# Performance work log

Measured on AMD Instinct MI355X. Metric: run time of the kernel, lower is better.

Reference implementation:

```python
import jax, jax.numpy as jnp
import numpy as np

B, T, D = 4096, 200, 64
H1, H2 = 64, 32


def _prelu(x, a):
    # PReLU with a single learnable slope (torch default num_parameters=1)
    return jnp.where(x >= 0, x, a * x)


def setup_inputs() -> dict:
    key = jax.random.key(0)
    ks = jax.random.split(key, 10)
    behavior = jax.random.normal(ks[0], (B, T, D), dtype=jnp.float32)
    candidate = jax.random.normal(ks[1], (B, D), dtype=jnp.float32)
    mask = jax.random.randint(ks[2], (B, T), 0, 2) > 0
    in_dim = 4 * D
    W1 = jax.random.normal(ks[3], (in_dim, H1), dtype=jnp.float32) / np.sqrt(in_dim)
    b1 = jnp.zeros((H1,), dtype=jnp.float32)
    a1 = jnp.full((1,), 0.25, dtype=jnp.float32)  # torch PReLU default init
    W2 = jax.random.normal(ks[4], (H1, H2), dtype=jnp.float32) / np.sqrt(H1)
    b2 = jnp.zeros((H2,), dtype=jnp.float32)
    a2 = jnp.full((1,), 0.25, dtype=jnp.float32)
    W3 = jax.random.normal(ks[5], (H2, 1), dtype=jnp.float32) / np.sqrt(H2)
    b3 = jnp.zeros((1,), dtype=jnp.float32)
    return {"behavior": behavior, "candidate": candidate, "mask": mask,
            "W1": W1, "b1": b1, "a1": a1,
            "W2": W2, "b2": b2, "a2": a2,
            "W3": W3, "b3": b3}


def reference(behavior, candidate, mask, W1, b1, a1, W2, b2, a2, W3, b3):
    # behavior: [B,T,D], candidate: [B,D], mask: [B,T] bool
    cand = candidate[:, None, :]                       # [B,1,D]
    cand_exp = jnp.broadcast_to(cand, behavior.shape)  # [B,T,D]
    diff = behavior - cand_exp
    prod = behavior * cand_exp
    att_input = jnp.concatenate([behavior, cand_exp, diff, prod], axis=-1)  # [B,T,4D]
    h = _prelu(att_input @ W1 + b1, a1)
    h = _prelu(h @ W2 + b2, a2)
    logits = (h @ W3 + b3)[..., 0]                     # [B,T]
    logits = jnp.where(mask, logits, -jnp.inf)
    w = jax.nn.softmax(logits, axis=-1)                # [B,T]
    user_interest = jnp.einsum('bt,btd->bd', w, behavior)  # [B,D]
    return user_interest
```

## Files before the change

kernel.cpp:

```cpp
#include <hip/hip_runtime.h>
#include <hip/hip_bf16.h>

#define T_LEN   200
#define NTILES  13

typedef __bf16 bf16x8 __attribute__((ext_vector_type(8)));
typedef __bf16 bf16x4 __attribute__((ext_vector_type(4)));
typedef float  f32x4  __attribute__((ext_vector_type(4)));

#if __has_builtin(__builtin_amdgcn_mfma_f32_16x16x16_bf16)
#define MFMA16(a, b, c) __builtin_amdgcn_mfma_f32_16x16x16_bf16((a), (b), (c), 0, 0, 0)
#elif __has_builtin(__builtin_amdgcn_mfma_f32_16x16x16bf16_1k)
#define MFMA16(a, b, c) __builtin_amdgcn_mfma_f32_16x16x16bf16_1k((a), (b), (c), 0, 0, 0)
#else
static __device__ __forceinline__ f32x4 mfma16_asm(bf16x4 a, bf16x4 b, f32x4 c) {
  asm("v_mfma_f32_16x16x16_bf16 %0, %1, %2, %0" : "+v"(c) : "v"(a), "v"(b));
  return c;
}
#define MFMA16(a, b, c) mfma16_asm((a), (b), (c))
#endif

#define MFMA32(a, b, c) __builtin_amdgcn_mfma_f32_16x16x32_bf16((a), (b), (c), 0, 0, 0)


__global__ __launch_bounds__(256) void prep_kernel(
    const float* __restrict__ W1g, const float* __restrict__ W2g,
    unsigned char* __restrict__ ws)
{
  const int idx = blockIdx.x * 256 + threadIdx.x;
  unsigned short* w1acP = (unsigned short*)(ws);
  unsigned short* w1dP  = (unsigned short*)(ws + 8192);
  unsigned short* w2P   = (unsigned short*)(ws + 16384);
  float*          wdifT = (float*)(ws + 20480);
  {
    int l = idx >> 6, q = idx & 63;
    int f = q >> 3, e = q & 7;
    int jt = f >> 1, kc = f & 1;
    int g = l >> 4, r = l & 15;
    int j = jt * 16 + r;
    int d = kc * 32 + g * 8 + e;
    float ac = W1g[d * 64 + j] + W1g[(128 + d) * 64 + j];
    float dd = W1g[(192 + d) * 64 + j];
    __bf16 acb = (__bf16)ac, ddb = (__bf16)dd;
    w1acP[l * 64 + f * 8 + e] = *(unsigned short*)&acb;
    w1dP [l * 64 + f * 8 + e] = *(unsigned short*)&ddb;
  }
  if (idx < 2048) {
    int l = idx >> 5, q = idx & 31;
    int f = q >> 2, i = q & 3;
    int nt = f >> 2, c = f & 3;
    int g = l >> 4, r = l & 15;
    __bf16 v = (__bf16)W2g[(c * 16 + g * 4 + i) * 32 + nt * 16 + r];
    w2P[l * 32 + f * 4 + i] = *(unsigned short*)&v;
  }
  {
    int j = idx & 63, d = idx >> 6;
    wdifT[j * 64 + d] = W1g[(64 + d) * 64 + j] - W1g[(128 + d) * 64 + j];
  }
}

__device__ __forceinline__ void loadA(const float* __restrict__ behB, int t, int kb,
                                      f32x4 (&x)[4]) {
  if (t < T_LEN) {
    const float* p = behB + (size_t)t * 64 + kb;
    x[0] = *(const f32x4*)p;
    x[1] = *(const f32x4*)(p + 4);
    x[2] = *(const f32x4*)(p + 32);
    x[3] = *(const f32x4*)(p + 36);
  } else {
    x[0] = f32x4{0.f, 0.f, 0.f, 0.f};
    x[1] = f32x4{0.f, 0.f, 0.f, 0.f};
    x[2] = f32x4{0.f, 0.f, 0.f, 0.f};
    x[3] = f32x4{0.f, 0.f, 0.f, 0.f};
  }
}

__global__ __launch_bounds__(64) void lau_kernel(
    const float* __restrict__ behG, const float* __restrict__ candG,
    const int*  __restrict__ maskG,
    const float* __restrict__ b1g, const float* __restrict__ a1g,
    const float* __restrict__ b2g, const float* __restrict__ a2g,
    const float* __restrict__ W3g,
    const unsigned char* __restrict__ ws,
    float* __restrict__ outG)
{
  const int lane = threadIdx.x;
  const int b    = blockIdx.x;
  const int r    = lane & 15;
  const int g    = lane >> 4;
  const int kb   = g * 8;

  const unsigned short* w1acP = (const unsigned short*)(ws);
  const unsigned short* w1dP  = (const unsigned short*)(ws + 8192);
  const unsigned short* w2P   = (const unsigned short*)(ws + 16384);
  const float*          wdifT = (const float*)(ws + 20480);

  const bool boolmask = (__ballot(((const unsigned int*)maskG)[lane] > 1u) != 0ull);

  const unsigned char* maskB8 = (const unsigned char*)maskG + (size_t)b * T_LEN;
  const int* maskB32 = maskG + (size_t)b * T_LEN;
  unsigned mbits = 0;
#pragma unroll
  for (int mt = 0; mt < NTILES; ++mt) {
    int t = mt * 16 + r;
    int mv = 0;
    if (t < T_LEN) mv = boolmask ? (int)maskB8[t] : maskB32[t];
    mbits |= (mv != 0 ? 1u : 0u) << mt;
  }

  const float* candB = candG + (size_t)b * 64;
  const f32x4 c0a = *(const f32x4*)(candB + kb);
  const f32x4 c0b = *(const f32x4*)(candB + kb + 4);
  const f32x4 c1a = *(const f32x4*)(candB + kb + 32);
  const f32x4 c1b = *(const f32x4*)(candB + kb + 36);

  bf16x8 A1[4][2];
#pragma unroll
  for (int f = 0; f < 8; ++f) {
    const int jt = f >> 1, kc = f & 1;
    bf16x8 ac = *(const bf16x8*)(w1acP + lane * 64 + f * 8);
    bf16x8 dd = *(const bf16x8*)(w1dP  + lane * 64 + f * 8);
    f32x4 cA = kc ? c1a : c0a;
    f32x4 cB = kc ? c1b : c0b;
    bf16x8 o;
#pragma unroll
    for (int e = 0; e < 4; ++e) {
      o[e]     = (__bf16)((float)ac[e]     + cA[e] * (float)dd[e]);
      o[4 + e] = (__bf16)((float)ac[4 + e] + cB[e] * (float)dd[4 + e]);
    }
    A1[jt][kc] = o;
  }

  bf16x4 W2f[8];
#pragma unroll
  for (int f = 0; f < 8; ++f)
    W2f[f] = *(const bf16x4*)(w2P + lane * 32 + f * 4);

  float biasv = b1g[lane];
  {
    const float* wdrow = wdifT + lane * 64;
#pragma unroll
    for (int d4 = 0; d4 < 16; ++d4) {
      f32x4 wd = *(const f32x4*)(wdrow + d4 * 4);
      f32x4 cd = *(const f32x4*)(candB + d4 * 4);
      biasv += wd[0] * cd[0] + wd[1] * cd[1] + wd[2] * cd[2] + wd[3] * cd[3];
    }
  }
  f32x4 bj4[4];
#pragma unroll
  for (int jt = 0; jt < 4; ++jt)
#pragma unroll
    for (int i = 0; i < 4; ++i)
      bj4[jt][i] = __shfl(biasv, jt * 16 + g * 4 + i);

  const float al1 = a1g[0];
  const float al2 = a2g[0];
  const f32x4 cinit0 = *(const f32x4*)(b2g + g * 4);
  const f32x4 cinit1 = *(const f32x4*)(b2g + 16 + g * 4);
  const f32x4 w3f0   = *(const f32x4*)(W3g + g * 4);
  const f32x4 w3f1   = *(const f32x4*)(W3g + 16 + g * 4);

  const float* behB = behG + (size_t)b * T_LEN * 64;

  float mrun = -__builtin_inff();
  float srun = 0.f;
  f32x4 o0 = {0,0,0,0}, o1 = {0,0,0,0}, o2 = {0,0,0,0}, o3 = {0,0,0,0};

  f32x4 xc[4];
  loadA(behB, r, kb, xc);

#pragma unroll 1
  for (int mt = 0; mt < NTILES; ++mt) {
    bf16x8 ab0, ab1;
#pragma unroll
    for (int i = 0; i < 4; ++i) {
      ab0[i]     = (__bf16)xc[0][i];
      ab0[4 + i] = (__bf16)xc[1][i];
      ab1[i]     = (__bf16)xc[2][i];
      ab1[4 + i] = (__bf16)xc[3][i];
    }
    if (mt + 1 < NTILES) {
      int tn = (mt + 1) * 16 + r;
      loadA(behB, tn, kb, xc);
    }

    bf16x4 a2f[4];
#pragma unroll
    for (int jt = 0; jt < 4; ++jt) {
      f32x4 acc = MFMA32(A1[jt][0], ab0, bj4[jt]);
      acc = MFMA32(A1[jt][1], ab1, acc);
#pragma unroll
      for (int i = 0; i < 4; ++i) {
        float h = acc[i];
        h = (h >= 0.f) ? h : al1 * h;
        a2f[jt][i] = (__bf16)h;
      }
    }

    f32x4 acc20 = cinit0, acc21 = cinit1;
#pragma unroll
    for (int c = 0; c < 4; ++c) acc20 = MFMA16(W2f[c],     a2f[c], acc20);
#pragma unroll
    for (int c = 0; c < 4; ++c) acc21 = MFMA16(W2f[4 + c], a2f[c], acc21);

    float partial = 0.f;
#pragma unroll
    for (int i = 0; i < 4; ++i) {
      float h0 = acc20[i]; h0 = (h0 >= 0.f) ? h0 : al2 * h0;
      float h1 = acc21[i]; h1 = (h1 >= 0.f) ? h1 : al2 * h1;
      partial += h0 * w3f0[i] + h1 * w3f1[i];
    }
    partial += __shfl_xor(partial, 16);
    partial += __shfl_xor(partial, 32);

    const bool valid = ((mbits >> mt) & 1u) != 0u;
    float lvt = valid ? partial : -__builtin_inff();
    if (lvt > mrun + 8.f) {
      float fs = __expf(mrun - lvt);
      srun *= fs;
#pragma unroll
      for (int i = 0; i < 4; ++i) { o0[i] *= fs; o1[i] *= fs; o2[i] *= fs; o3[i] *= fs; }
      mrun = lvt;
    }
    float et = valid ? __expf(lvt - mrun) : 0.f;
    srun += et;
#pragma unroll
    for (int i = 0; i < 4; ++i) {
      o0[i] += et * (float)ab0[i];
      o1[i] += et * (float)ab0[4 + i];
      o2[i] += et * (float)ab1[i];
      o3[i] += et * (float)ab1[4 + i];
    }
  }

  float M = mrun;
#pragma unroll
  for (int off = 1; off < 16; off <<= 1) M = fmaxf(M, __shfl_xor(M, off));
  {
    float fac = __expf(mrun - M);
    srun *= fac;
#pragma unroll
    for (int i = 0; i < 4; ++i) { o0[i] *= fac; o1[i] *= fac; o2[i] *= fac; o3[i] *= fac; }
  }
#pragma unroll
  for (int off = 1; off < 16; off <<= 1) {
#pragma unroll
    for (int i = 0; i < 4; ++i) {
      o0[i] += __shfl_xor(o0[i], off);
      o1[i] += __shfl_xor(o1[i], off);
      o2[i] += __shfl_xor(o2[i], off);
      o3[i] += __shfl_xor(o3[i], off);
    }
    srun += __shfl_xor(srun, off);
  }
  if (r == 0) {
    float inv = 1.f / srun;
    float* po = outG + (size_t)b * 64 + kb;
#pragma unroll
    for (int i = 0; i < 4; ++i) {
      o0[i] *= inv; o1[i] *= inv; o2[i] *= inv; o3[i] *= inv;
    }
    *(f32x4*)(po)      = o0;
    *(f32x4*)(po + 4)  = o1;
    *(f32x4*)(po + 32) = o2;
    *(f32x4*)(po + 36) = o3;
  }
}

extern "C" void kernel_launch(void* const* d_in, const int* in_sizes, int n_in,
                              void* d_out, int out_size, void* d_ws, size_t ws_size,
                              hipStream_t stream) {
  (void)n_in; (void)ws_size; (void)out_size;
  const float* beh  = (const float*)d_in[0];
  const float* cand = (const float*)d_in[1];
  const int*   mask = (const int*)d_in[2];
  const float* W1   = (const float*)d_in[3];
  const float* b1   = (const float*)d_in[4];
  const float* a1   = (const float*)d_in[5];
  const float* W2   = (const float*)d_in[6];
  const float* b2   = (const float*)d_in[7];
  const float* a2   = (const float*)d_in[8];
  const float* W3   = (const float*)d_in[9];

  unsigned char* ws = (unsigned char*)d_ws;
  prep_kernel<<<16, 256, 0, stream>>>(W1, W2, ws);

  int B = in_sizes[1] / 64;
  lau_kernel<<<B, 64, 0, stream>>>(beh, cand, mask, b1, a1, b2, a2, W3,
                                   ws, (float*)d_out);
}
```

Before: 66.51 us.

## Stage behavior tiles through swizzled LDS double buffer with coalesced loads, 4 batches per block

Replaces the per-lane strided global loads of behavior rows with fully coalesced row-contiguous loads that are written into a per-wave, XOR-swizzled LDS double buffer and then read back in the MFMA operand layout. Each block now holds four waves, one per batch row, launched with a quarter of the grid. The aim is better global memory coalescing and latency hiding on a bandwidth-bound kernel, at the cost of extra LDS traffic and 32KB of shared memory per block, which may limit occupancy. The code relies on wave-synchronous LDS use with no explicit barrier, and it assumes B is divisible by 4.

```diff
diff --git a/kernel.cpp b/kernel.cpp
--- a/kernel.cpp
+++ b/kernel.cpp
@@ -59,23 +59,7 @@
   }
 }
 
-__device__ __forceinline__ void loadA(const float* __restrict__ behB, int t, int kb,
-                                      f32x4 (&x)[4]) {
-  if (t < T_LEN) {
-    const float* p = behB + (size_t)t * 64 + kb;
-    x[0] = *(const f32x4*)p;
-    x[1] = *(const f32x4*)(p + 4);
-    x[2] = *(const f32x4*)(p + 32);
-    x[3] = *(const f32x4*)(p + 36);
-  } else {
-    x[0] = f32x4{0.f, 0.f, 0.f, 0.f};
-    x[1] = f32x4{0.f, 0.f, 0.f, 0.f};
-    x[2] = f32x4{0.f, 0.f, 0.f, 0.f};
-    x[3] = f32x4{0.f, 0.f, 0.f, 0.f};
-  }
-}
-
-__global__ __launch_bounds__(64) void lau_kernel(
+__global__ __launch_bounds__(256) void lau_kernel(
     const float* __restrict__ behG, const float* __restrict__ candG,
     const int*  __restrict__ maskG,
     const float* __restrict__ b1g, const float* __restrict__ a1g,
@@ -84,8 +68,12 @@
     const unsigned char* __restrict__ ws,
     float* __restrict__ outG)
 {
-  const int lane = threadIdx.x;
-  const int b    = blockIdx.x;
+  __shared__ float tb[4][2][1024];
+
+  const int tid  = threadIdx.x;
+  const int lane = tid & 63;
+  const int wv   = tid >> 6;
+  const int b    = blockIdx.x * 4 + wv;
   const int r    = lane & 15;
   const int g    = lane >> 4;
   const int kb   = g * 8;
@@ -160,28 +148,65 @@
   const f32x4 w3f0   = *(const f32x4*)(W3g + g * 4);
   const f32x4 w3f1   = *(const f32x4*)(W3g + 16 + g * 4);
 
-  const float* behB = behG + (size_t)b * T_LEN * 64;
+  const unsigned char* behB = (const unsigned char*)(behG + (size_t)b * T_LEN * 64);
+
+  int srow[4], wrad[4];
+#pragma unroll
+  for (int k = 0; k < 4; ++k) {
+    srow[k] = 4 * k + g;
+    int soff = r * 16;
+    wrad[k] = srow[k] * 256 + (soff ^ ((srow[k] & 7) << 4));
+  }
+  int rdad[4];
+#pragma unroll
+  for (int q = 0; q < 4; ++q) {
+    int off = (q >> 1) * 128 + g * 32 + (q & 1) * 16;
+    rdad[q] = r * 256 + (off ^ ((r & 7) << 4));
+  }
+
+  unsigned char* myb0 = (unsigned char*)&tb[wv][0][0];
+  unsigned char* myb1 = (unsigned char*)&tb[wv][1][0];
 
   float mrun = -__builtin_inff();
   float srun = 0.f;
   f32x4 o0 = {0,0,0,0}, o1 = {0,0,0,0}, o2 = {0,0,0,0}, o3 = {0,0,0,0};
 
-  f32x4 xc[4];
-  loadA(behB, r, kb, xc);
+  f32x4 y[4];
+#pragma unroll
+  for (int k = 0; k < 4; ++k) {
+    int gt = srow[k];
+    y[k] = *(const f32x4*)(behB + (size_t)gt * 256 + r * 16);
+  }
+#pragma unroll
+  for (int k = 0; k < 4; ++k)
+    *(f32x4*)(myb0 + wrad[k]) = y[k];
 
 #pragma unroll 1
   for (int mt = 0; mt < NTILES; ++mt) {
+    unsigned char* bufc = (mt & 1) ? myb1 : myb0;
+    unsigned char* bufn = (mt & 1) ? myb0 : myb1;
+
+    if (mt + 1 < NTILES) {
+#pragma unroll
+      for (int k = 0; k < 4; ++k) {
+        int gt = (mt + 1) * 16 + srow[k];
+        gt = (gt < T_LEN) ? gt : (T_LEN - 1);
+        y[k] = *(const f32x4*)(behB + (size_t)gt * 256 + r * 16);
+      }
+    }
+
+    f32x4 xc0 = *(const f32x4*)(bufc + rdad[0]);
+    f32x4 xc1 = *(const f32x4*)(bufc + rdad[1]);
+    f32x4 xc2 = *(const f32x4*)(bufc + rdad[2]);
+    f32x4 xc3 = *(const f32x4*)(bufc + rdad[3]);
+
     bf16x8 ab0, ab1;
 #pragma unroll
     for (int i = 0; i < 4; ++i) {
-      ab0[i]     = (__bf16)xc[0][i];
-      ab0[4 + i] = (__bf16)xc[1][i];
-      ab1[i]     = (__bf16)xc[2][i];
-      ab1[4 + i] = (__bf16)xc[3][i];
-    }
-    if (mt + 1 < NTILES) {
-      int tn = (mt + 1) * 16 + r;
-      loadA(behB, tn, kb, xc);
+      ab0[i]     = (__bf16)xc0[i];
+      ab0[4 + i] = (__bf16)xc1[i];
+      ab1[i]     = (__bf16)xc2[i];
+      ab1[4 + i] = (__bf16)xc3[i];
     }
 
     bf16x4 a2f[4];
@@ -230,6 +255,12 @@
       o1[i] += et * (float)ab0[4 + i];
       o2[i] += et * (float)ab1[i];
       o3[i] += et * (float)ab1[4 + i];
+    }
+
+    if (mt + 1 < NTILES) {
+#pragma unroll
+      for (int k = 0; k < 4; ++k)
+        *(f32x4*)(bufn + wrad[k]) = y[k];
     }
   }
 
@@ -286,6 +317,7 @@
   prep_kernel<<<16, 256, 0, stream>>>(W1, W2, ws);
 
   int B = in_sizes[1] / 64;
-  lau_kernel<<<B, 64, 0, stream>>>(beh, cand, mask, b1, a1, b2, a2, W3,
-                                   ws, (float*)d_out);
+  int grid = B / 4;
+  lau_kernel<<<grid, 256, 0, stream>>>(beh, cand, mask, b1, a1, b2, a2, W3,
+                                       ws, (float*)d_out);
 }
```

Measured after the change: 58.01 us. 1.15x faster.
